# Kernel optimization log

Measured on AMD Instinct MI355X. Metric: run time of the kernel, lower is better.

Reference implementation:

```python
import jax, jax.numpy as jnp
import numpy as np

B, H, W = 8, 256, 256
ALPHA = 1.0
BETA = 1.0
EPS = 1e-06
_INF = 1e10  # stands in for +inf in fp32 min-plus EDT


def _minplus_1d(f):
    """Exact 1D squared-distance transform along the last axis.
    g[..., i] = min_j ( f[..., j] + (i - j)^2 )."""
    n = f.shape[-1]
    i = jnp.arange(n)
    D = ((i[:, None] - i[None, :]) ** 2).astype(f.dtype)  # [n, n]
    # broadcast: [..., 1, n] + [n, n] -> [..., n, n] -> min over j
    return jnp.min(f[..., None, :] + D, axis=-1)


def _edt(binary):
    """Exact Euclidean distance to the nearest zero element of `binary`
    (matches scipy.ndimage.distance_transform_edt). binary: [..., H, W]."""
    f = jnp.where(binary > 0.5, _INF, 0.0)
    g = _minplus_1d(f)                         # pass along W
    h = _minplus_1d(jnp.swapaxes(g, -1, -2))   # pass along H
    return jnp.sqrt(jnp.swapaxes(h, -1, -2))


def setup_inputs() -> dict:
    key = jax.random.key(0)
    k1, k2 = jax.random.split(key)
    pred = jax.random.normal(k1, (B, 1, H, W), dtype=jnp.float32)
    target = jax.random.randint(k2, (B, 1, H, W), 0, 2).astype(jnp.float32)
    return {"pred": pred, "target": target, "from_logits": 1}


def reference(pred, target, from_logits):
    if from_logits:
        pred = jax.nn.sigmoid(pred)
    # dice loss
    intersection = 2.0 * jnp.sum(pred * target, axis=(1, 2, 3))
    union = jnp.sum(pred ** 2, axis=(1, 2, 3)) + jnp.sum(target ** 2, axis=(1, 2, 3))
    d_loss = jnp.mean(1.0 - (intersection + EPS) / (union + EPS))
    # boundary loss: dist_out (EDT of ~mask) + dist_in (EDT of mask), no grad
    t = jax.lax.stop_gradient(target[:, 0])  # [B, H, W]
    dist_map = _edt(1.0 - t) + _edt(t)        # [B, H, W]
    b_loss = jnp.mean(pred * dist_map[:, None, :, :])
    return ALPHA * d_loss + BETA * b_loss
```

## Files before the change

### kernel.cpp

```cpp
#include <hip/hip_runtime.h>
#include <math.h>

#define BB 8
#define HH 256
#define WW 256
#define NROW (BB*HH)
#define NCOL (BB*WW)
#define EPSF 1e-6f
#define INFV 1e10f


__global__ __launch_bounds__(256) void k_rowpass(
    const float* __restrict__ pred, const float* __restrict__ target,
    const int* __restrict__ from_logits,
    uint2* __restrict__ gsp, float* __restrict__ part)
{
    const int row = blockIdx.x;
    const int b   = row >> 8;
    const int r   = row & 255;
    const int c   = threadIdx.x;
    const int base = row * WW;

    __shared__ float trow[WW];
    const float t = target[base + c];
    const float p = pred[base + c];
    const float sp = (*from_logits) ? (1.0f / (1.0f + __expf(-p))) : p;
    trow[c] = t;
    __syncthreads();

    const bool isone = (t > 0.5f);
    float best1 = isone ? 0.0f : INFV;
    float best0 = isone ? INFV : 0.0f;
    for (int d = 1; d < WW; ++d) {
        const float dd = (float)(d * d);
        if (dd >= best0 && dd >= best1) break;
        const int l = c - d, rr = c + d;
        if (l >= 0) {
            if (trow[l] > 0.5f) best1 = fminf(best1, dd);
            else                best0 = fminf(best0, dd);
        }
        if (rr < WW) {
            if (trow[rr] > 0.5f) best1 = fminf(best1, dd);
            else                best0 = fminf(best0, dd);
        }
    }
    const unsigned u1 = (best1 > 65500.0f) ? 0xFFFFu : (unsigned)best1;
    const unsigned u0 = (best0 > 65500.0f) ? 0xFFFFu : (unsigned)best0;
    uint2 rec;
    rec.x = u1 | (u0 << 16);
    rec.y = __float_as_uint(sp);
    gsp[(b * WW + c) * HH + r] = rec;

    float s_pt = sp * t;
    float s_p2 = sp * sp;
    float s_t  = t * t;
    #pragma unroll
    for (int o = 32; o > 0; o >>= 1) {
        s_pt += __shfl_down(s_pt, o);
        s_p2 += __shfl_down(s_p2, o);
        s_t  += __shfl_down(s_t,  o);
    }
    __shared__ float red[12];
    const int lane = c & 63, wid = c >> 6;
    if (lane == 0) { red[wid] = s_pt; red[4 + wid] = s_p2; red[8 + wid] = s_t; }
    __syncthreads();
    if (c == 0) {
        part[row]            = red[0] + red[1] + red[2] + red[3];
        part[NROW + row]     = red[4] + red[5] + red[6] + red[7];
        part[2 * NROW + row] = red[8] + red[9] + red[10] + red[11];
    }
}

__global__ __launch_bounds__(256) void k_colpass(
    const uint2* __restrict__ gsp, float* __restrict__ part_pd)
{
    const int blk = blockIdx.x;
    const int r   = threadIdx.x;

    __shared__ float c1[HH], c0[HH];
    const uint2 rec = gsp[blk * HH + r];
    const unsigned u1 = rec.x & 0xFFFFu, u0 = rec.x >> 16;
    const float f1 = (u1 == 0xFFFFu) ? INFV : (float)u1;
    const float f0 = (u0 == 0xFFFFu) ? INFV : (float)u0;
    const float sp = __uint_as_float(rec.y);
    c1[r] = f1; c0[r] = f0;
    __syncthreads();

    float best1 = f1;
    float best0 = f0;
    for (int d = 1; d < HH; ++d) {
        const float dd = (float)(d * d);
        if (dd >= best0 && dd >= best1) break;
        const int u = r - d, v = r + d;
        if (u >= 0) {
            best1 = fminf(best1, c1[u] + dd);
            best0 = fminf(best0, c0[u] + dd);
        }
        if (v < HH) {
            best1 = fminf(best1, c1[v] + dd);
            best0 = fminf(best0, c0[v] + dd);
        }
    }
    float s_pd = sp * (sqrtf(best1) + sqrtf(best0));

    #pragma unroll
    for (int o = 32; o > 0; o >>= 1) s_pd += __shfl_down(s_pd, o);
    __shared__ float red[4];
    const int lane = r & 63, wid = r >> 6;
    if (lane == 0) red[wid] = s_pd;
    __syncthreads();
    if (r == 0) part_pd[blk] = red[0] + red[1] + red[2] + red[3];
}

__global__ __launch_bounds__(256) void k_final(
    const float* __restrict__ part, float* __restrict__ out)
{
    const int t = threadIdx.x;

    float s = 0.0f;
    for (int i = t; i < NCOL; i += 256) s += part[3 * NROW + i];
    #pragma unroll
    for (int o = 32; o > 0; o >>= 1) s += __shfl_down(s, o);
    __shared__ float bsum[4];
    if ((t & 63) == 0) bsum[t >> 6] = s;

    const int b = t >> 5, j = t & 31;
    float pt = 0.0f, p2 = 0.0f, st = 0.0f;
    for (int k = j; k < HH; k += 32) {
        const int idx = b * HH + k;
        pt += part[idx];
        p2 += part[NROW + idx];
        st += part[2 * NROW + idx];
    }
    #pragma unroll
    for (int o = 16; o > 0; o >>= 1) {
        pt += __shfl_down(pt, o, 32);
        p2 += __shfl_down(p2, o, 32);
        st += __shfl_down(st, o, 32);
    }
    __shared__ float dice[8];
    if (j == 0) dice[b] = 1.0f - (2.0f * pt + EPSF) / (p2 + st + EPSF);
    __syncthreads();

    if (t == 0) {
        float dsum = 0.0f;
        #pragma unroll
        for (int bb = 0; bb < 8; ++bb) dsum += dice[bb];
        const float b_loss = (bsum[0] + bsum[1] + bsum[2] + bsum[3])
                             / (float)(BB * HH * WW);
        out[0] = dsum / (float)BB + b_loss;
    }
}

extern "C" void kernel_launch(void* const* d_in, const int* in_sizes, int n_in,
                              void* d_out, int out_size, void* d_ws, size_t ws_size,
                              hipStream_t stream) {
    const float* pred   = (const float*)d_in[0];
    const float* target = (const float*)d_in[1];
    const int*   fl     = (const int*)d_in[2];
    float* out = (float*)d_out;

    float* part = (float*)d_ws;
    uint2* gsp  = (uint2*)((char*)d_ws + 32 * 1024);

    k_rowpass<<<NROW, 256, 0, stream>>>(pred, target, fl, gsp, part);
    k_colpass<<<NCOL, 256, 0, stream>>>(gsp, part + 3 * NROW);
    k_final<<<1, 256, 0, stream>>>(part, out);
}
```

Measured before the change: 74.40 us.

## Process four rows per rowpass block and fuse final reduction via last-block atomic

The row pass now gives each block four consecutive rows, so every thread writes its four transposed records as two 16-byte stores instead of four scattered 8-byte stores, and there are fewer blocks. The separate final kernel is removed: each column-pass block publishes its partial sum, bumps an atomic counter, and the last block to finish does the global reduction. This removes one kernel launch and improves write coalescing into the transposed buffer. The cost is fewer row-pass blocks (512) with more serial work each, plus a fence and atomic per column block. The counter is reset in the row pass, which relies on ordering between the two kernels.

```diff
diff --git a/kernel.cpp b/kernel.cpp
--- a/kernel.cpp
+++ b/kernel.cpp
@@ -4,8 +4,8 @@
 #define BB 8
 #define HH 256
 #define WW 256
-#define NROW (BB*HH)
-#define NCOL (BB*WW)
+#define NBLKR 512
+#define NCOL  2048
 #define EPSF 1e-6f
 #define INFV 1e10f
 
@@ -15,45 +15,57 @@
     const int* __restrict__ from_logits,
     uint2* __restrict__ gsp, float* __restrict__ part)
 {
-    const int row = blockIdx.x;
-    const int b   = row >> 8;
-    const int r   = row & 255;
+    const int blk = blockIdx.x;
+    const int b   = blk >> 6;
+    const int r0  = (blk & 63) << 2;
     const int c   = threadIdx.x;
-    const int base = row * WW;
+    const int gbase = (b * HH + r0) * WW;
 
-    __shared__ float trow[WW];
-    const float t = target[base + c];
-    const float p = pred[base + c];
-    const float sp = (*from_logits) ? (1.0f / (1.0f + __expf(-p))) : p;
-    trow[c] = t;
+    __shared__ float trow[4][WW];
+    float tv[4], sp[4];
+    const int fl = *from_logits;
+    #pragma unroll
+    for (int k = 0; k < 4; ++k) {
+        const float t = target[gbase + k * WW + c];
+        const float p = pred[gbase + k * WW + c];
+        trow[k][c] = t;
+        tv[k] = t;
+        sp[k] = fl ? (1.0f / (1.0f + __expf(-p))) : p;
+    }
     __syncthreads();
 
-    const bool isone = (t > 0.5f);
-    float best1 = isone ? 0.0f : INFV;
-    float best0 = isone ? INFV : 0.0f;
-    for (int d = 1; d < WW; ++d) {
-        const float dd = (float)(d * d);
-        if (dd >= best0 && dd >= best1) break;
-        const int l = c - d, rr = c + d;
-        if (l >= 0) {
-            if (trow[l] > 0.5f) best1 = fminf(best1, dd);
-            else                best0 = fminf(best0, dd);
+    float s_pt = 0.0f, s_p2 = 0.0f, s_t = 0.0f;
+    unsigned xs[4], ys[4];
+    #pragma unroll
+    for (int k = 0; k < 4; ++k) {
+        const bool isone = (tv[k] > 0.5f);
+        float best1 = isone ? 0.0f : INFV;
+        float best0 = isone ? INFV : 0.0f;
+        for (int d = 1; d < WW; ++d) {
+            const float dd = (float)(d * d);
+            if (dd >= best0 && dd >= best1) break;
+            const int l = c - d, rr = c + d;
+            if (l >= 0) {
+                if (trow[k][l] > 0.5f) best1 = fminf(best1, dd);
+                else                   best0 = fminf(best0, dd);
+            }
+            if (rr < WW) {
+                if (trow[k][rr] > 0.5f) best1 = fminf(best1, dd);
+                else                    best0 = fminf(best0, dd);
+            }
         }
-        if (rr < WW) {
-            if (trow[rr] > 0.5f) best1 = fminf(best1, dd);
-            else                best0 = fminf(best0, dd);
-        }
+        const unsigned u1 = (best1 > 65500.0f) ? 0xFFFFu : (unsigned)best1;
+        const unsigned u0 = (best0 > 65500.0f) ? 0xFFFFu : (unsigned)best0;
+        xs[k] = u1 | (u0 << 16);
+        ys[k] = __float_as_uint(sp[k]);
+        s_pt += sp[k] * tv[k];
+        s_p2 += sp[k] * sp[k];
+        s_t  += tv[k] * tv[k];
     }
-    const unsigned u1 = (best1 > 65500.0f) ? 0xFFFFu : (unsigned)best1;
-    const unsigned u0 = (best0 > 65500.0f) ? 0xFFFFu : (unsigned)best0;
-    uint2 rec;
-    rec.x = u1 | (u0 << 16);
-    rec.y = __float_as_uint(sp);
-    gsp[(b * WW + c) * HH + r] = rec;
+    uint4* dst = (uint4*)&gsp[(b * WW + c) * HH + r0];
+    dst[0] = make_uint4(xs[0], ys[0], xs[1], ys[1]);
+    dst[1] = make_uint4(xs[2], ys[2], xs[3], ys[3]);
 
-    float s_pt = sp * t;
-    float s_p2 = sp * sp;
-    float s_t  = t * t;
     #pragma unroll
     for (int o = 32; o > 0; o >>= 1) {
         s_pt += __shfl_down(s_pt, o);
@@ -65,14 +77,16 @@
     if (lane == 0) { red[wid] = s_pt; red[4 + wid] = s_p2; red[8 + wid] = s_t; }
     __syncthreads();
     if (c == 0) {
-        part[row]            = red[0] + red[1] + red[2] + red[3];
-        part[NROW + row]     = red[4] + red[5] + red[6] + red[7];
-        part[2 * NROW + row] = red[8] + red[9] + red[10] + red[11];
+        part[blk]        = red[0] + red[1] + red[2] + red[3];
+        part[512 + blk]  = red[4] + red[5] + red[6] + red[7];
+        part[1024 + blk] = red[8] + red[9] + red[10] + red[11];
+        if (blk == 0) ((unsigned*)part)[3584] = 0u;
     }
 }
 
 __global__ __launch_bounds__(256) void k_colpass(
-    const uint2* __restrict__ gsp, float* __restrict__ part_pd)
+    const uint2* __restrict__ gsp, float* __restrict__ part,
+    float* __restrict__ out)
 {
     const int blk = blockIdx.x;
     const int r   = threadIdx.x;
@@ -86,8 +100,7 @@
     c1[r] = f1; c0[r] = f0;
     __syncthreads();
 
-    float best1 = f1;
-    float best0 = f0;
+    float best1 = f1, best0 = f0;
     for (int d = 1; d < HH; ++d) {
         const float dd = (float)(d * d);
         if (dd >= best0 && dd >= best1) break;
@@ -105,20 +118,25 @@
 
     #pragma unroll
     for (int o = 32; o > 0; o >>= 1) s_pd += __shfl_down(s_pd, o);
-    __shared__ float red[4];
+    __shared__ float redf[4];
     const int lane = r & 63, wid = r >> 6;
-    if (lane == 0) red[wid] = s_pd;
+    if (lane == 0) redf[wid] = s_pd;
     __syncthreads();
-    if (r == 0) part_pd[blk] = red[0] + red[1] + red[2] + red[3];
-}
 
-__global__ __launch_bounds__(256) void k_final(
-    const float* __restrict__ part, float* __restrict__ out)
-{
-    const int t = threadIdx.x;
+    __shared__ int amLast;
+    if (r == 0) {
+        part[1536 + blk] = redf[0] + redf[1] + redf[2] + redf[3];
+        __threadfence();
+        const unsigned old = atomicAdd(&((unsigned*)part)[3584], 1u);
+        amLast = (old == (unsigned)(NCOL - 1));
+    }
+    __syncthreads();
+    if (!amLast) return;
+    __threadfence();
 
+    const int t = r;
     float s = 0.0f;
-    for (int i = t; i < NCOL; i += 256) s += part[3 * NROW + i];
+    for (int i = t; i < NCOL; i += 256) s += part[1536 + i];
     #pragma unroll
     for (int o = 32; o > 0; o >>= 1) s += __shfl_down(s, o);
     __shared__ float bsum[4];
@@ -126,11 +144,11 @@
 
     const int b = t >> 5, j = t & 31;
     float pt = 0.0f, p2 = 0.0f, st = 0.0f;
-    for (int k = j; k < HH; k += 32) {
-        const int idx = b * HH + k;
+    for (int k = j; k < 64; k += 32) {
+        const int idx = b * 64 + k;
         pt += part[idx];
-        p2 += part[NROW + idx];
-        st += part[2 * NROW + idx];
+        p2 += part[512 + idx];
+        st += part[1024 + idx];
     }
     #pragma unroll
     for (int o = 16; o > 0; o >>= 1) {
@@ -163,7 +181,6 @@
     float* part = (float*)d_ws;
     uint2* gsp  = (uint2*)((char*)d_ws + 32 * 1024);
 
-    k_rowpass<<<NROW, 256, 0, stream>>>(pred, target, fl, gsp, part);
-    k_colpass<<<NCOL, 256, 0, stream>>>(gsp, part + 3 * NROW);
-    k_final<<<1, 256, 0, stream>>>(part, out);
+    k_rowpass<<<NBLKR, 256, 0, stream>>>(pred, target, fl, gsp, part);
+    k_colpass<<<NCOL, 256, 0, stream>>>(gsp, part, out);
 }
```

After: 111.8 us. 1.5x slower.

## Fuse row and column EDT passes into one kernel using bitmask nearest-distance

Applied to the files above, without the earlier changes.

Replaces the separate row-pass and column-pass kernels with a single kernel. Each of 64 blocks loads a whole batch image's target as a packed bitmask in shared memory. Row distances come from ctz/clz bit scans instead of a linear search, are kept as 8-bit values for the block's 32-column strip, and the column pass then runs out of shared memory. This removes the global intermediate transpose buffer and one launch. The trade-off is that only 64 blocks of 512 threads run, so parallelism is much lower, and every block redundantly builds the full-image mask.

```diff
diff --git a/kernel.cpp b/kernel.cpp
--- a/kernel.cpp
+++ b/kernel.cpp
@@ -4,152 +4,188 @@
 #define BB 8
 #define HH 256
 #define WW 256
-#define NROW (BB*HH)
-#define NCOL (BB*WW)
+#define SW 32
+#define NBLK (BB*8)
+#define NT 512
 #define EPSF 1e-6f
-#define INFV 1e10f
-
-
-__global__ __launch_bounds__(256) void k_rowpass(
+
+__device__ __forceinline__ int nearest_dist(const unsigned long long* m, int c)
+{
+    const int w = c >> 6, o = c & 63;
+    int dr = 256;
+    const unsigned long long right = m[w] >> o;
+    if (right) dr = __builtin_ctzll(right);
+    else {
+        for (int ww = w + 1; ww < 4; ++ww)
+            if (m[ww]) { dr = (ww - w) * 64 - o + __builtin_ctzll(m[ww]); break; }
+    }
+    int dl = 256;
+    const unsigned long long left = m[w] << (63 - o);
+    if (left) dl = __builtin_clzll(left);
+    else {
+        for (int ww = w - 1; ww >= 0; --ww)
+            if (m[ww]) { dl = o + 1 + (w - ww - 1) * 64 + __builtin_clzll(m[ww]); break; }
+    }
+    const int n = dr < dl ? dr : dl;
+    return n < 255 ? n : 255;
+}
+
+__global__ __launch_bounds__(NT) void k_fused(
     const float* __restrict__ pred, const float* __restrict__ target,
-    const int* __restrict__ from_logits,
-    uint2* __restrict__ gsp, float* __restrict__ part)
+    const int* __restrict__ from_logits, float* __restrict__ part)
 {
-    const int row = blockIdx.x;
-    const int b   = row >> 8;
-    const int r   = row & 255;
-    const int c   = threadIdx.x;
-    const int base = row * WW;
-
-    __shared__ float trow[WW];
-    const float t = target[base + c];
-    const float p = pred[base + c];
-    const float sp = (*from_logits) ? (1.0f / (1.0f + __expf(-p))) : p;
-    trow[c] = t;
+    __shared__ unsigned char maskb[HH * 68];
+    __shared__ unsigned char gbuf[HH * 72];
+    __shared__ float red[32];
+
+    const int blk = blockIdx.x;
+    const int b   = blk >> 3;
+    const int c0  = (blk & 7) * SW;
+    const int t   = threadIdx.x;
+    const int fl  = *from_logits;
+    const float* tb = target + b * HH * WW;
+    const float* pb = pred   + b * HH * WW;
+
+    {
+        const float4* t4 = (const float4*)tb;
+        #pragma unroll 4
+        for (int i = 0; i < 32; ++i) {
+            const int f = i * NT + t;
+            const float4 v = t4[f];
+            const int row = f >> 6;
+            const int q   = f & 63;
+            const unsigned nib = (v.x > 0.5f ? 1u : 0u) | (v.y > 0.5f ? 2u : 0u)
+                               | (v.z > 0.5f ? 4u : 0u) | (v.w > 0.5f ? 8u : 0u);
+            maskb[row * 68 + q] = (unsigned char)nib;
+        }
+    }
     __syncthreads();
 
-    const bool isone = (t > 0.5f);
-    float best1 = isone ? 0.0f : INFV;
-    float best0 = isone ? INFV : 0.0f;
-    for (int d = 1; d < WW; ++d) {
-        const float dd = (float)(d * d);
-        if (dd >= best0 && dd >= best1) break;
-        const int l = c - d, rr = c + d;
-        if (l >= 0) {
-            if (trow[l] > 0.5f) best1 = fminf(best1, dd);
-            else                best0 = fminf(best0, dd);
-        }
-        if (rr < WW) {
-            if (trow[rr] > 0.5f) best1 = fminf(best1, dd);
-            else                best0 = fminf(best0, dd);
-        }
-    }
-    const unsigned u1 = (best1 > 65500.0f) ? 0xFFFFu : (unsigned)best1;
-    const unsigned u0 = (best0 > 65500.0f) ? 0xFFFFu : (unsigned)best0;
-    uint2 rec;
-    rec.x = u1 | (u0 << 16);
-    rec.y = __float_as_uint(sp);
-    gsp[(b * WW + c) * HH + r] = rec;
-
-    float s_pt = sp * t;
-    float s_p2 = sp * sp;
-    float s_t  = t * t;
+    {
+        const int row = t >> 1;
+        const int k0  = (t & 1) * 16;
+        const unsigned char* mb = maskb + row * 68;
+        unsigned long long m[4];
+        #pragma unroll
+        for (int w = 0; w < 4; ++w) {
+            unsigned long long acc = 0ull;
+            #pragma unroll
+            for (int j = 0; j < 4; ++j) {
+                unsigned x = *(const unsigned*)(mb + (w * 4 + j) * 4);
+                x = (x | (x >> 4)) & 0x00FF00FFu;
+                x = (x | (x >> 8)) & 0x0000FFFFu;
+                acc |= ((unsigned long long)x) << (16 * j);
+            }
+            m[w] = acc;
+        }
+        const unsigned long long mi[4] = { ~m[0], ~m[1], ~m[2], ~m[3] };
+        for (int kk = k0; kk < k0 + 16; kk += 4) {
+            unsigned lo = 0, hi = 0;
+            #pragma unroll
+            for (int j = 0; j < 4; ++j) {
+                const int c  = c0 + kk + j;
+                const unsigned n1 = (unsigned)nearest_dist(m,  c);
+                const unsigned n0 = (unsigned)nearest_dist(mi, c);
+                const unsigned pv = n1 | (n0 << 8);
+                if (j < 2) lo |= pv << (16 * j);
+                else       hi |= pv << (16 * (j - 2));
+            }
+            *(uint2*)(gbuf + row * 72 + kk * 2) = make_uint2(lo, hi);
+        }
+    }
+    __syncthreads();
+
+    float s_pt = 0.0f, s_p2 = 0.0f, s_st = 0.0f, s_bd = 0.0f;
+    {
+        const int k  = t & 31;
+        const int c  = c0 + k;
+        const int r0 = (t >> 5) * 16;
+        float pv[16];
+        #pragma unroll
+        for (int rr = 0; rr < 16; ++rr) pv[rr] = pb[(r0 + rr) * WW + c];
+
+        #pragma unroll 4
+        for (int rr = 0; rr < 16; ++rr) {
+            const int r = r0 + rr;
+            const float p  = pv[rr];
+            const float sp = fl ? (1.0f / (1.0f + __expf(-p))) : p;
+            const unsigned short vc = *(const unsigned short*)(gbuf + r * 72 + 2 * k);
+            const int n1 = vc & 255, n0 = vc >> 8;
+            int best1 = n1 * n1, best0 = n0 * n0;
+            for (int d = 1;; ++d) {
+                const int dd = d * d;
+                if (dd >= best1 && dd >= best0) break;
+                const int u = r - d, v2 = r + d;
+                if (u >= 0) {
+                    const unsigned short vu = *(const unsigned short*)(gbuf + u * 72 + 2 * k);
+                    const int a = vu & 255, bq = vu >> 8;
+                    best1 = min(best1, a * a + dd);
+                    best0 = min(best0, bq * bq + dd);
+                }
+                if (v2 < HH) {
+                    const unsigned short vd = *(const unsigned short*)(gbuf + v2 * 72 + 2 * k);
+                    const int a = vd & 255, bq = vd >> 8;
+                    best1 = min(best1, a * a + dd);
+                    best0 = min(best0, bq * bq + dd);
+                }
+            }
+            const float dist = sqrtf((float)best1) + sqrtf((float)best0);
+            const int bit = (maskb[r * 68 + (c >> 2)] >> (c & 3)) & 1;
+            const float tv = (float)bit;
+            s_pt += sp * tv;
+            s_p2 += sp * sp;
+            s_st += tv;
+            s_bd += sp * dist;
+        }
+    }
+
     #pragma unroll
     for (int o = 32; o > 0; o >>= 1) {
         s_pt += __shfl_down(s_pt, o);
         s_p2 += __shfl_down(s_p2, o);
-        s_t  += __shfl_down(s_t,  o);
-    }
-    __shared__ float red[12];
-    const int lane = c & 63, wid = c >> 6;
-    if (lane == 0) { red[wid] = s_pt; red[4 + wid] = s_p2; red[8 + wid] = s_t; }
+        s_st += __shfl_down(s_st, o);
+        s_bd += __shfl_down(s_bd, o);
+    }
+    const int lane = t & 63, wid = t >> 6;
+    if (lane == 0) {
+        red[wid] = s_pt; red[8 + wid] = s_p2;
+        red[16 + wid] = s_st; red[24 + wid] = s_bd;
+    }
     __syncthreads();
-    if (c == 0) {
-        part[row]            = red[0] + red[1] + red[2] + red[3];
-        part[NROW + row]     = red[4] + red[5] + red[6] + red[7];
-        part[2 * NROW + row] = red[8] + red[9] + red[10] + red[11];
-    }
-}
-
-__global__ __launch_bounds__(256) void k_colpass(
-    const uint2* __restrict__ gsp, float* __restrict__ part_pd)
-{
-    const int blk = blockIdx.x;
-    const int r   = threadIdx.x;
-
-    __shared__ float c1[HH], c0[HH];
-    const uint2 rec = gsp[blk * HH + r];
-    const unsigned u1 = rec.x & 0xFFFFu, u0 = rec.x >> 16;
-    const float f1 = (u1 == 0xFFFFu) ? INFV : (float)u1;
-    const float f0 = (u0 == 0xFFFFu) ? INFV : (float)u0;
-    const float sp = __uint_as_float(rec.y);
-    c1[r] = f1; c0[r] = f0;
-    __syncthreads();
-
-    float best1 = f1;
-    float best0 = f0;
-    for (int d = 1; d < HH; ++d) {
-        const float dd = (float)(d * d);
-        if (dd >= best0 && dd >= best1) break;
-        const int u = r - d, v = r + d;
-        if (u >= 0) {
-            best1 = fminf(best1, c1[u] + dd);
-            best0 = fminf(best0, c0[u] + dd);
-        }
-        if (v < HH) {
-            best1 = fminf(best1, c1[v] + dd);
-            best0 = fminf(best0, c0[v] + dd);
-        }
-    }
-    float s_pd = sp * (sqrtf(best1) + sqrtf(best0));
-
-    #pragma unroll
-    for (int o = 32; o > 0; o >>= 1) s_pd += __shfl_down(s_pd, o);
-    __shared__ float red[4];
-    const int lane = r & 63, wid = r >> 6;
-    if (lane == 0) red[wid] = s_pd;
-    __syncthreads();
-    if (r == 0) part_pd[blk] = red[0] + red[1] + red[2] + red[3];
-}
-
-__global__ __launch_bounds__(256) void k_final(
+    if (t == 0) {
+        float a = 0, bb2 = 0, cc = 0, dd = 0;
+        #pragma unroll
+        for (int w = 0; w < 8; ++w) {
+            a  += red[w];      bb2 += red[8 + w];
+            cc += red[16 + w]; dd  += red[24 + w];
+        }
+        part[blk * 4 + 0] = a;  part[blk * 4 + 1] = bb2;
+        part[blk * 4 + 2] = cc; part[blk * 4 + 3] = dd;
+    }
+}
+
+__global__ __launch_bounds__(64) void k_final(
     const float* __restrict__ part, float* __restrict__ out)
 {
     const int t = threadIdx.x;
-
-    float s = 0.0f;
-    for (int i = t; i < NCOL; i += 256) s += part[3 * NROW + i];
+    float pt = part[t * 4 + 0], p2 = part[t * 4 + 1];
+    float st = part[t * 4 + 2], bd = part[t * 4 + 3];
     #pragma unroll
-    for (int o = 32; o > 0; o >>= 1) s += __shfl_down(s, o);
-    __shared__ float bsum[4];
-    if ((t & 63) == 0) bsum[t >> 6] = s;
-
-    const int b = t >> 5, j = t & 31;
-    float pt = 0.0f, p2 = 0.0f, st = 0.0f;
-    for (int k = j; k < HH; k += 32) {
-        const int idx = b * HH + k;
-        pt += part[idx];
-        p2 += part[NROW + idx];
-        st += part[2 * NROW + idx];
-    }
+    for (int o = 4; o > 0; o >>= 1) {
+        pt += __shfl_down(pt, o, 8);
+        p2 += __shfl_down(p2, o, 8);
+        st += __shfl_down(st, o, 8);
+        bd += __shfl_down(bd, o, 8);
+    }
+    float dice = ((t & 7) == 0) ? (1.0f - (2.0f * pt + EPSF) / (p2 + st + EPSF)) : 0.0f;
+    float bdv  = ((t & 7) == 0) ? bd : 0.0f;
     #pragma unroll
-    for (int o = 16; o > 0; o >>= 1) {
-        pt += __shfl_down(pt, o, 32);
-        p2 += __shfl_down(p2, o, 32);
-        st += __shfl_down(st, o, 32);
-    }
-    __shared__ float dice[8];
-    if (j == 0) dice[b] = 1.0f - (2.0f * pt + EPSF) / (p2 + st + EPSF);
-    __syncthreads();
-
-    if (t == 0) {
-        float dsum = 0.0f;
-        #pragma unroll
-        for (int bb = 0; bb < 8; ++bb) dsum += dice[bb];
-        const float b_loss = (bsum[0] + bsum[1] + bsum[2] + bsum[3])
-                             / (float)(BB * HH * WW);
-        out[0] = dsum / (float)BB + b_loss;
-    }
+    for (int o = 8; o < 64; o <<= 1) {
+        dice += __shfl_down(dice, o);
+        bdv  += __shfl_down(bdv, o);
+    }
+    if (t == 0)
+        out[0] = dice / (float)BB + bdv / (float)(BB * HH * WW);
 }
 
 extern "C" void kernel_launch(void* const* d_in, const int* in_sizes, int n_in,
@@ -158,12 +194,9 @@
     const float* pred   = (const float*)d_in[0];
     const float* target = (const float*)d_in[1];
     const int*   fl     = (const int*)d_in[2];
-    float* out = (float*)d_out;
-
+    float* out  = (float*)d_out;
     float* part = (float*)d_ws;
-    uint2* gsp  = (uint2*)((char*)d_ws + 32 * 1024);
-
-    k_rowpass<<<NROW, 256, 0, stream>>>(pred, target, fl, gsp, part);
-    k_colpass<<<NCOL, 256, 0, stream>>>(gsp, part + 3 * NROW);
-    k_final<<<1, 256, 0, stream>>>(part, out);
-}
+
+    k_fused<<<NBLK, NT, 0, stream>>>(pred, target, fl, part);
+    k_final<<<1, 64, 0, stream>>>(part, out);
+}
```

After: 77.93 us. +4.8%, slower.
